# Optimization experiments

Measured on AMD Instinct MI355X. Metric: run time of the kernel, lower is better.

The kernel has to match this reference:

```python
import jax, jax.numpy as jnp
import numpy as np

B, L, D, C = 8, 1024, 512, 4  # batch, maxlen, input_units(=output_unit), channel


def setup_inputs() -> dict:
    key = jax.random.key(0)
    ks = jax.random.split(key, 6)
    scale = 1.0 / np.sqrt(D)  # glorot-ish
    inputs = jax.random.normal(ks[0], (B, L, D), dtype=jnp.float32)
    pad_k = jnp.zeros((B, L, 1), dtype=jnp.float32)  # 0 = valid, -99999 = pad
    w_l = jax.random.normal(ks[1], (C, D, D), dtype=jnp.float32) * scale   # scalar_w per channel
    b_l = jnp.zeros((C,), dtype=jnp.float32)                                # scalar_b per channel
    w_v1 = jax.random.normal(ks[2], (C, D), dtype=jnp.float32) * scale     # vector_w1 [D,1] squeezed
    w_v2 = jax.random.normal(ks[3], (C, D, D), dtype=jnp.float32) * scale  # vector_w2
    b_v = jnp.zeros((C, D), dtype=jnp.float32)                              # vector_b [1,1,D] squeezed
    return {"inputs": inputs, "pad_k": pad_k, "w_l": w_l, "b_l": b_l,
            "w_v1": w_v1, "w_v2": w_v2, "b_v": b_v}


def reference(inputs, pad_k, w_l, b_l, w_v1, w_v2, b_v):
    # inputs: [B,L,D], pad_k: [B,L,1]. Dropout (mask_prob) is identity at inference.
    pad_k2 = (pad_k + 99999.0) / 99999.0              # [B,L,1], 1 at valid, 0 at pad
    pk = pad_k[:, None, :, 0]                          # [B,1,L]

    # --- scalar (pairwise bilinear) attention, all channels at once ---
    mat_l = jnp.einsum('bld,cde->bcle', inputs, w_l)   # [B,C,L,D]
    # M[b,c,i,j] = sum_d inputs[b,i,d] * mat_l[b,c,j,d] + b_l[c]
    M = jnp.einsum('bid,bcjd->bcij', inputs, mat_l) + b_l[None, :, None, None]
    A = jnp.tanh(M)                                    # [B,C,L,L]
    s = A.sum(axis=3)                                  # sum over j -> [B,C,L]
    a = jax.nn.softmax(pk + s, axis=-1)[..., None]     # softmax over L -> [B,C,L,1]

    # --- vector attention ---
    sb = jnp.tanh(jnp.einsum('bld,cde->bcle', inputs, w_v2) + b_v[None, :, None, :])  # [B,C,L,D]
    score_bar = jnp.einsum('bcld,cd->bcl', sb, w_v1) + pk                              # [B,C,L]
    a_bar = jax.nn.softmax(score_bar, axis=-1)                                         # [B,C,L]
    pooled = jnp.einsum('bcl,bld->bcd', a_bar, inputs)                                 # [B,C,D]

    # C_l = a_l * inputs + pooled(broadcast over L) * pad_k2
    C_l = a * inputs[:, None] + pooled[:, :, None, :] * pad_k2[:, None]                # [B,C,L,D]

    C_features = jnp.concatenate(
        [jnp.transpose(C_l, (0, 2, 3, 1)), inputs[..., None]], axis=-1)                # [B,L,D,C+1]
    return C_features, a, a_bar[..., None]
```

## Files before the change

### kernel.cpp

```cpp
#include <hip/hip_runtime.h>

#define BB 8
#define LL 1024
#define DD 512
#define CC 4

typedef unsigned short u16;
typedef unsigned int u32;
typedef __attribute__((ext_vector_type(8))) short bf16x8;
typedef __attribute__((ext_vector_type(4))) float f32x4;
typedef __attribute__((ext_vector_type(4))) unsigned short u16x4;
typedef __attribute__((ext_vector_type(4))) float float4v;

typedef __attribute__((address_space(1))) const u32 gu32;
typedef __attribute__((address_space(3))) u32 lu32;
typedef __attribute__((address_space(3))) u16 l16;

__device__ __forceinline__ void gload16(const void* g, void* l) {
  __builtin_amdgcn_global_load_lds((gu32*)g, (lu32*)l, 16, 0, 0);
}
__device__ __forceinline__ u32 lds_off(const u16* p) {
  return (u32)(uintptr_t)(l16*)p;
}

__device__ __forceinline__ u16 f2bf(float f) {
  unsigned u = __float_as_uint(f);
  u += 0x7FFF + ((u >> 16) & 1);
  return (u16)(u >> 16);
}
__device__ __forceinline__ float bf2f(u16 h) {
  return __uint_as_float(((unsigned)h) << 16);
}
__device__ __forceinline__ float fast_tanh(float x) {
  return 1.0f - 2.0f / (__expf(2.0f * x) + 1.0f);
}

__global__ __launch_bounds__(256) void k_split(const float4v* __restrict__ x,
                                               u16* __restrict__ hi, u16* __restrict__ lo) {
  int i = blockIdx.x * 256 + threadIdx.x;
  float4v v = x[i];
  u16x4 h, l;
#pragma unroll
  for (int k = 0; k < 4; ++k) {
    u16 hh = f2bf(v[k]);
    h[k] = hh;
    l[k] = f2bf(v[k] - bf2f(hh));
  }
  *(u16x4*)&hi[(size_t)i * 4] = h;
  *(u16x4*)&lo[(size_t)i * 4] = l;
}

__global__ __launch_bounds__(256) void k_tsplit(const float* __restrict__ w,
                                                u16* __restrict__ thi, u16* __restrict__ tlo) {
  __shared__ float t[32][33];
  int c = blockIdx.z;
  int tx = threadIdx.x;
  int ty = threadIdx.y;
  int e0 = blockIdx.x * 32, d0 = blockIdx.y * 32;
#pragma unroll
  for (int k = 0; k < 32; k += 8)
    t[ty + k][tx] = w[((size_t)c * DD + d0 + ty + k) * DD + e0 + tx];
  __syncthreads();
#pragma unroll
  for (int k = 0; k < 32; k += 8) {
    float v = t[tx][ty + k];
    size_t o = ((size_t)c * DD + e0 + ty + k) * DD + d0 + tx;
    u16 h = f2bf(v);
    thi[o] = h;
    if (tlo) tlo[o] = f2bf(v - bf2f(h));
  }
}

#define DSR(dst, addr, OFF) \
  asm volatile("ds_read_b128 %0, %1 offset:" #OFF : "=v"(dst) : "v"(addr))
#define LGKM(N) \
  do { __builtin_amdgcn_sched_barrier(0); \
       asm volatile("s_waitcnt lgkmcnt(" #N ")" ::: "memory"); \
       __builtin_amdgcn_sched_barrier(0); } while (0)

template<int NSEG, bool SPLIT>
__device__ __forceinline__ void gemm256(const u16* __restrict__ Ahi, const u16* __restrict__ Alo,
                                        const u16* __restrict__ Bhi, const u16* __restrict__ Blo,
                                        u16* lA, u16* lB, f32x4 (&acc)[8][4]) {
  const int tid = threadIdx.x;
  const int lane = tid & 63;
  const int wave = tid >> 6;
  const int wr = wave >> 2, wc = wave & 3;
  const int fr = lane & 15;
  const int fq = lane >> 4;
  const int srow = tid >> 2;
  const int xs = (tid & 3) ^ ((srow >> 1) & 3);
  const size_t soff = (size_t)srow * DD + (size_t)xs * 8;
  const int sidx = fq ^ ((fr >> 1) & 3);
  const u32 ra = lds_off(lA) + (u32)((wr * 128 + fr) * 64 + sidx * 16);
  const u32 rb = lds_off(lB) + (u32)((wc * 64 + fr) * 64 + sidx * 16);

  const int NT = NSEG * 16;

#define STAGE(t, beo) do {                                                    \
    const int seg_ = SPLIT ? ((t) >> 4) : 0;                                  \
    const int kp_ = ((t) & 15) * 32;                                          \
    const u16* As_ = (SPLIT && seg_ == 1) ? Alo : Ahi;                        \
    const u16* Bs_ = (SPLIT && seg_ == 2) ? Blo : Bhi;                        \
    _Pragma("unroll")                                                         \
    for (int i_ = 0; i_ < 2; ++i_) {                                          \
      gload16(As_ + soff + (size_t)i_ * 128 * DD + kp_,                       \
              lA + (beo) + tid * 8 + i_ * 4096);                              \
      gload16(Bs_ + soff + (size_t)i_ * 128 * DD + kp_,                       \
              lB + (beo) + tid * 8 + i_ * 4096);                              \
    }                                                                         \
  } while (0)

#define MFMA2(m0, m1) do {                                                    \
    _Pragma("unroll")                                                         \
    for (int ni = 0; ni < 4; ++ni)                                            \
      acc[m0][ni] = __builtin_amdgcn_mfma_f32_16x16x32_bf16(                  \
          af[m0], bv[ni], acc[m0][ni], 0, 0, 0);                              \
    _Pragma("unroll")                                                         \
    for (int ni = 0; ni < 4; ++ni)                                            \
      acc[m1][ni] = __builtin_amdgcn_mfma_f32_16x16x32_bf16(                  \
          af[m1], bv[ni], acc[m1][ni], 0, 0, 0);                              \
  } while (0)

#define COMPUTE(bo_) do {                                                     \
    u32 aA_ = ra + (bo_), aB_ = rb + (bo_);                                   \
    bf16x8 af[8], bv[4];                                                      \
    DSR(bv[0], aB_, 0);    DSR(bv[1], aB_, 1024);                             \
    DSR(bv[2], aB_, 2048); DSR(bv[3], aB_, 3072);                             \
    DSR(af[0], aA_, 0);    DSR(af[1], aA_, 1024);                             \
    DSR(af[2], aA_, 2048); DSR(af[3], aA_, 3072);                             \
    LGKM(2);                         \
    __builtin_amdgcn_s_setprio(1);                                            \
    MFMA2(0, 1);                                                              \
    DSR(af[4], aA_, 4096); DSR(af[5], aA_, 5120);                             \
    LGKM(2);                                \
    MFMA2(2, 3);                                                              \
    DSR(af[6], aA_, 6144); DSR(af[7], aA_, 7168);                             \
    LGKM(2);                                \
    MFMA2(4, 5);                                                              \
    LGKM(0);                              \
    MFMA2(6, 7);                                                              \
    __builtin_amdgcn_s_setprio(0);                                            \
    __builtin_amdgcn_s_barrier();            \
  } while (0)

  STAGE(0, 0);
  STAGE(1, 8192);
  int be = 16384;
  u32 bo = 0;
#pragma unroll 1
  for (int t = 0; t < NT - 2; ++t) {
    STAGE(t + 2, be);
    be = (be == 16384) ? 0 : be + 8192;
    __builtin_amdgcn_sched_barrier(0);
    asm volatile("s_waitcnt vmcnt(8)" ::: "memory");
    __builtin_amdgcn_sched_barrier(0);
    __builtin_amdgcn_s_barrier();
    __builtin_amdgcn_sched_barrier(0);
    COMPUTE(bo);
    bo = (bo == 32768u) ? 0u : bo + 16384u;
  }
  __builtin_amdgcn_sched_barrier(0);
  asm volatile("s_waitcnt vmcnt(4)" ::: "memory");
  __builtin_amdgcn_sched_barrier(0);
  __builtin_amdgcn_s_barrier();
  __builtin_amdgcn_sched_barrier(0);
  COMPUTE(bo);
  bo = (bo == 32768u) ? 0u : bo + 16384u;
  __builtin_amdgcn_sched_barrier(0);
  asm volatile("s_waitcnt vmcnt(0)" ::: "memory");
  __builtin_amdgcn_sched_barrier(0);
  __builtin_amdgcn_s_barrier();
  __builtin_amdgcn_sched_barrier(0);
  COMPUTE(bo);
#undef STAGE
#undef COMPUTE
#undef MFMA2
}

__global__ __launch_bounds__(512, 2) void k_matl(const u16* __restrict__ Xhi, const u16* __restrict__ Xlo,
                                                 const u16* __restrict__ Whi, const u16* __restrict__ Wlo,
                                                 u16* __restrict__ mhi, u16* __restrict__ mlo) {
  __shared__ u16 lA[3 * 256 * 32];
  __shared__ u16 lB[3 * 256 * 32];
  int lin = blockIdx.x;
  int virt = (lin & 7) * 32 + (lin >> 3);
  int bc = virt >> 3, rem = virt & 7;
  int tm = rem >> 1, tn = rem & 1;
  int b = bc >> 2, c = bc & 3;
  const u16* Ahi = Xhi + (size_t)b * LL * DD + (size_t)tm * 256 * DD;
  const u16* Alo = Xlo + (size_t)b * LL * DD + (size_t)tm * 256 * DD;
  const u16* Bhi = Whi + (size_t)c * DD * DD + (size_t)tn * 256 * DD;
  const u16* Blo = Wlo + (size_t)c * DD * DD + (size_t)tn * 256 * DD;
  f32x4 acc[8][4];
#pragma unroll
  for (int mi = 0; mi < 8; ++mi)
#pragma unroll
    for (int ni = 0; ni < 4; ++ni) acc[mi][ni] = (f32x4){0.f, 0.f, 0.f, 0.f};
  gemm256<3, true>(Ahi, Alo, Bhi, Blo, lA, lB, acc);

  int lane = threadIdx.x & 63, wave = threadIdx.x >> 6;
  int wr = wave >> 2, wc = wave & 3;
  int rgrp = (lane >> 4) * 4, cidx = lane & 15;
#pragma unroll
  for (int mi = 0; mi < 8; ++mi)
#pragma unroll
    for (int ni = 0; ni < 4; ++ni) {
      int row = tm * 256 + wr * 128 + mi * 16 + rgrp;
      int col = tn * 256 + wc * 64 + ni * 16 + cidx;
#pragma unroll
      for (int j = 0; j < 4; ++j) {
        float v = acc[mi][ni][j];
        size_t o = ((size_t)bc * LL + row + j) * DD + col;
        u16 h = f2bf(v);
        mhi[o] = h;
        mlo[o] = f2bf(v - bf2f(h));
      }
    }
}

__global__ __launch_bounds__(512, 2) void k_s(const u16* __restrict__ Xhi, const u16* __restrict__ Xlo,
                                              const u16* __restrict__ mhi, const u16* __restrict__ mlo,
                                              const float* __restrict__ b_l, float* __restrict__ s_part) {
  __shared__ u16 lA[3 * 256 * 32];
  __shared__ u16 lB[3 * 256 * 32];
  int lin = blockIdx.x;
  int virt = (lin & 7) * 64 + (lin >> 3);
  int bc = virt >> 4, rem = virt & 15;
  int tm = rem >> 2, tn = rem & 3;
  int b = bc >> 2, c = bc & 3;
  const u16* Ahi = Xhi + (size_t)b * LL * DD + (size_t)tm * 256 * DD;
  const u16* Alo = Xlo + (size_t)b * LL * DD + (size_t)tm * 256 * DD;
  const u16* Bhi = mhi + (size_t)bc * LL * DD + (size_t)tn * 256 * DD;
  const u16* Blo = mlo + (size_t)bc * LL * DD + (size_t)tn * 256 * DD;
  f32x4 acc[8][4];
#pragma unroll
  for (int mi = 0; mi < 8; ++mi)
#pragma unroll
    for (int ni = 0; ni < 4; ++ni) acc[mi][ni] = (f32x4){0.f, 0.f, 0.f, 0.f};
  gemm256<3, true>(Ahi, Alo, Bhi, Blo, lA, lB, acc);

  int lane = threadIdx.x & 63, wave = threadIdx.x >> 6;
  int wr = wave >> 2, wc = wave & 3;
  float bl = b_l[c];
  float part[8][4];
#pragma unroll
  for (int mi = 0; mi < 8; ++mi)
#pragma unroll
    for (int j = 0; j < 4; ++j) part[mi][j] = 0.f;
#pragma unroll
  for (int mi = 0; mi < 8; ++mi)
#pragma unroll
    for (int ni = 0; ni < 4; ++ni)
#pragma unroll
      for (int j = 0; j < 4; ++j) part[mi][j] += fast_tanh(acc[mi][ni][j] + bl);
#pragma unroll
  for (int mi = 0; mi < 8; ++mi)
#pragma unroll
    for (int j = 0; j < 4; ++j) {
      float v = part[mi][j];
      v += __shfl_xor(v, 1, 64);
      v += __shfl_xor(v, 2, 64);
      v += __shfl_xor(v, 4, 64);
      v += __shfl_xor(v, 8, 64);
      part[mi][j] = v;
    }
  if ((lane & 15) == 0) {
    int slot = bc * 16 + tn * 4 + wc;
    int rg = (lane >> 4) * 4;
#pragma unroll
    for (int mi = 0; mi < 8; ++mi)
#pragma unroll
      for (int j = 0; j < 4; ++j) {
        int row = tm * 256 + wr * 128 + mi * 16 + rg + j;
        s_part[(size_t)slot * LL + row] = part[mi][j];
      }
  }
}

__global__ __launch_bounds__(512, 2) void k_sbar(const u16* __restrict__ Xhi, const u16* __restrict__ Wv2T,
                                                 const float* __restrict__ b_v, const float* __restrict__ w_v1,
                                                 float* __restrict__ sc_part) {
  __shared__ u16 lA[3 * 256 * 32];
  __shared__ u16 lB[3 * 256 * 32];
  int lin = blockIdx.x;
  int virt = (lin & 7) * 32 + (lin >> 3);
  int bc = virt >> 3, rem = virt & 7;
  int tm = rem >> 1, tn = rem & 1;
  int b = bc >> 2, c = bc & 3;
  const u16* Ahi = Xhi + (size_t)b * LL * DD + (size_t)tm * 256 * DD;
  const u16* Bhi = Wv2T + (size_t)c * DD * DD + (size_t)tn * 256 * DD;
  f32x4 acc[8][4];
#pragma unroll
  for (int mi = 0; mi < 8; ++mi)
#pragma unroll
    for (int ni = 0; ni < 4; ++ni) acc[mi][ni] = (f32x4){0.f, 0.f, 0.f, 0.f};
  gemm256<1, false>(Ahi, nullptr, Bhi, nullptr, lA, lB, acc);

  int lane = threadIdx.x & 63, wave = threadIdx.x >> 6;
  int wr = wave >> 2, wc = wave & 3;
  int cidx = lane & 15;
  float wv[4], bvv[4];
#pragma unroll
  for (int ni = 0; ni < 4; ++ni) {
    int col = tn * 256 + wc * 64 + ni * 16 + cidx;
    wv[ni] = w_v1[c * DD + col];
    bvv[ni] = b_v[c * DD + col];
  }
  float part[8][4];
#pragma unroll
  for (int mi = 0; mi < 8; ++mi)
#pragma unroll
    for (int j = 0; j < 4; ++j) part[mi][j] = 0.f;
#pragma unroll
  for (int mi = 0; mi < 8; ++mi)
#pragma unroll
    for (int ni = 0; ni < 4; ++ni)
#pragma unroll
      for (int j = 0; j < 4; ++j) part[mi][j] += fast_tanh(acc[mi][ni][j] + bvv[ni]) * wv[ni];
#pragma unroll
  for (int mi = 0; mi < 8; ++mi)
#pragma unroll
    for (int j = 0; j < 4; ++j) {
      float v = part[mi][j];
      v += __shfl_xor(v, 1, 64);
      v += __shfl_xor(v, 2, 64);
      v += __shfl_xor(v, 4, 64);
      v += __shfl_xor(v, 8, 64);
      part[mi][j] = v;
    }
  if ((lane & 15) == 0) {
    int slot = bc * 8 + tn * 4 + wc;
    int rg = (lane >> 4) * 4;
#pragma unroll
    for (int mi = 0; mi < 8; ++mi)
#pragma unroll
      for (int j = 0; j < 4; ++j) {
        int row = tm * 256 + wr * 128 + mi * 16 + rg + j;
        sc_part[(size_t)slot * LL + row] = part[mi][j];
      }
  }
}

__device__ __forceinline__ float blk_max(float v, float* red, int tid) {
#pragma unroll
  for (int m = 32; m >= 1; m >>= 1) v = fmaxf(v, __shfl_xor(v, m, 64));
  if ((tid & 63) == 0) red[tid >> 6] = v;
  __syncthreads();
  float r = red[0];
#pragma unroll
  for (int k = 1; k < 16; ++k) r = fmaxf(r, red[k]);
  __syncthreads();
  return r;
}
__device__ __forceinline__ float blk_sum(float v, float* red, int tid) {
#pragma unroll
  for (int m = 32; m >= 1; m >>= 1) v += __shfl_xor(v, m, 64);
  if ((tid & 63) == 0) red[tid >> 6] = v;
  __syncthreads();
  float r = red[0];
#pragma unroll
  for (int k = 1; k < 16; ++k) r += red[k];
  __syncthreads();
  return r;
}

__global__ __launch_bounds__(1024) void k_softmax(const float* __restrict__ s_part,
                                                  const float* __restrict__ sc_part,
                                                  const float* __restrict__ pad_k,
                                                  const float* __restrict__ X,
                                                  float* __restrict__ a_out,
                                                  float* __restrict__ abar_out,
                                                  float* __restrict__ pooled) {
  __shared__ float red[16];
  __shared__ float sm_abar[LL];
  __shared__ float pp[DD];
  int bc = blockIdx.x, b = bc >> 2;
  int i = threadIdx.x;
  float pk = pad_k[b * LL + i];

  float s = pk;
#pragma unroll
  for (int p = 0; p < 16; ++p) s += s_part[(size_t)(bc * 16 + p) * LL + i];
  float mx = blk_max(s, red, i);
  float e = expf(s - mx);
  float sum = blk_sum(e, red, i);
  float a = e / sum;
  a_out[bc * LL + i] = a;

  float sb = pk;
#pragma unroll
  for (int p = 0; p < 8; ++p) sb += sc_part[(size_t)(bc * 8 + p) * LL + i];
  float mx2 = blk_max(sb, red, i);
  float e2 = expf(sb - mx2);
  float sum2 = blk_sum(e2, red, i);
  float ab = e2 / sum2;
  abar_out[bc * LL + i] = ab;
  sm_abar[i] = ab;
  __syncthreads();

  {
    int d = i & (DD - 1), h = i >> 9;
    const float* xb = X + (size_t)b * LL * DD + (size_t)h * 512 * DD + d;
    const float* abp = sm_abar + h * 512;
    float a0 = 0.f, a1 = 0.f, a2 = 0.f, a3 = 0.f;
    for (int l = 0; l < 512; l += 4) {
      a0 += abp[l + 0] * xb[(size_t)(l + 0) * DD];
      a1 += abp[l + 1] * xb[(size_t)(l + 1) * DD];
      a2 += abp[l + 2] * xb[(size_t)(l + 2) * DD];
      a3 += abp[l + 3] * xb[(size_t)(l + 3) * DD];
    }
    float sv = (a0 + a1) + (a2 + a3);
    if (h == 1) pp[d] = sv;
    __syncthreads();
    if (h == 0) pooled[bc * DD + d] = sv + pp[d];
  }
}

__global__ __launch_bounds__(256) void k_assemble(const float* __restrict__ X,
                                                  const float* __restrict__ pad_k,
                                                  const float* __restrict__ a,
                                                  const float* __restrict__ pooled,
                                                  float* __restrict__ out) {
  __shared__ float buf[1280];
  int t = threadIdx.x;
  size_t idx = (size_t)blockIdx.x * 256 + t;
  int d = (int)(idx & (DD - 1));
  int bl = (int)(idx >> 9);
  int b = bl >> 10;
  int l = bl & (LL - 1);
  float x = X[idx];
  float pk2 = (pad_k[bl] + 99999.0f) * (1.0f / 99999.0f);
#pragma unroll
  for (int c = 0; c < 4; ++c) {
    float av = a[(size_t)(b * 4 + c) * LL + l];
    float pv = pooled[(size_t)(b * 4 + c) * DD + d];
    buf[t * 5 + c] = av * x + pv * pk2;
  }
  buf[t * 5 + 4] = x;
  __syncthreads();
  size_t base = (size_t)blockIdx.x * 1280;
#pragma unroll
  for (int k = 0; k < 5; ++k) out[base + k * 256 + t] = buf[k * 256 + t];
}

extern "C" void kernel_launch(void* const* d_in, const int* in_sizes, int n_in,
                              void* d_out, int out_size, void* d_ws, size_t ws_size,
                              hipStream_t stream) {
  (void)in_sizes; (void)n_in; (void)out_size;
  const float* X     = (const float*)d_in[0];
  const float* pad_k = (const float*)d_in[1];
  const float* w_l   = (const float*)d_in[2];
  const float* b_l   = (const float*)d_in[3];
  const float* w_v1  = (const float*)d_in[4];
  const float* w_v2  = (const float*)d_in[5];
  const float* b_v   = (const float*)d_in[6];
  float* out = (float*)d_out;

  char* wsp = (char*)d_ws;
  const size_t NEED = 26279936;
  bool small_ws = ws_size < NEED;
  u16* Xhi = (u16*)wsp;
  u16* Xlo = small_ws ? (u16*)((char*)d_out + 67108864)
                      : (u16*)(wsp + 8388608);
  size_t off = small_ws ? 8388608 : 16777216;
  u16* WlThi = (u16*)(wsp + off);  off += 2097152;
  u16* WlTlo = (u16*)(wsp + off);  off += 2097152;
  u16* Wv2T  = (u16*)(wsp + off);  off += 2097152;
  float* s_part  = (float*)(wsp + off); off += 2097152;
  float* sc_part = (float*)(wsp + off); off += 1048576;
  float* pooled  = (float*)(wsp + off); off += 65536;

  u16* mhi = (u16*)d_out;
  u16* mlo = (u16*)d_out + 16777216;

  float* a_out    = out + 20971520;
  float* abar_out = out + 21004288;

  k_split<<<4096, 256, 0, stream>>>((const float4v*)X, Xhi, Xlo);
  k_tsplit<<<dim3(16, 16, 4), dim3(32, 8), 0, stream>>>(w_l, WlThi, WlTlo);
  k_tsplit<<<dim3(16, 16, 4), dim3(32, 8), 0, stream>>>(w_v2, Wv2T, nullptr);

  k_matl<<<256, 512, 0, stream>>>(Xhi, Xlo, WlThi, WlTlo, mhi, mlo);
  k_s<<<512, 512, 0, stream>>>(Xhi, Xlo, mhi, mlo, b_l, s_part);
  k_sbar<<<256, 512, 0, stream>>>(Xhi, Wv2T, b_v, w_v1, sc_part);

  k_softmax<<<32, 1024, 0, stream>>>(s_part, sc_part, pad_k, X, a_out, abar_out, pooled);
  k_assemble<<<16384, 256, 0, stream>>>(X, pad_k, a_out, pooled, out);
}
```

Before: 244.3 us.

## Interleave half of GEMM prefetch with MFMAs and split pooling into parallel kernel

The GEMM main loop now issues only half of each stage's global-to-LDS loads before the barrier and the other half in the middle of the MFMA sequence. The wait count is adjusted to match, so load issue overlaps with matrix compute instead of bunching up at the top of each iteration. Separately, the attention-weighted pooling over L is moved out of the 32-block softmax kernel into its own 256-block kernel, which spreads the strided reads of X over many more CUs. The cost is one extra kernel launch and a round trip of a_bar through global memory.

```diff
diff --git a/kernel.cpp b/kernel.cpp
--- a/kernel.cpp
+++ b/kernel.cpp
@@ -97,18 +97,15 @@
 
   const int NT = NSEG * 16;
 
-#define STAGE(t, beo) do {                                                    \
+#define STAGE_PAIR(t, beo, half) do {                                         \
     const int seg_ = SPLIT ? ((t) >> 4) : 0;                                  \
     const int kp_ = ((t) & 15) * 32;                                          \
     const u16* As_ = (SPLIT && seg_ == 1) ? Alo : Ahi;                        \
     const u16* Bs_ = (SPLIT && seg_ == 2) ? Blo : Bhi;                        \
-    _Pragma("unroll")                                                         \
-    for (int i_ = 0; i_ < 2; ++i_) {                                          \
-      gload16(As_ + soff + (size_t)i_ * 128 * DD + kp_,                       \
-              lA + (beo) + tid * 8 + i_ * 4096);                              \
-      gload16(Bs_ + soff + (size_t)i_ * 128 * DD + kp_,                       \
-              lB + (beo) + tid * 8 + i_ * 4096);                              \
-    }                                                                         \
+    gload16(As_ + soff + (size_t)(half) * 128 * DD + kp_,                     \
+            lA + (beo) + tid * 8 + (half) * 4096);                            \
+    gload16(Bs_ + soff + (size_t)(half) * 128 * DD + kp_,                     \
+            lB + (beo) + tid * 8 + (half) * 4096);                            \
   } while (0)
 
 #define MFMA2(m0, m1) do {                                                    \
@@ -122,42 +119,63 @@
           af[m1], bv[ni], acc[m1][ni], 0, 0, 0);                              \
   } while (0)
 
-#define COMPUTE(bo_) do {                                                     \
+#define COMPUTE_PEEL(bo_) do {                                                \
     u32 aA_ = ra + (bo_), aB_ = rb + (bo_);                                   \
     bf16x8 af[8], bv[4];                                                      \
     DSR(bv[0], aB_, 0);    DSR(bv[1], aB_, 1024);                             \
     DSR(bv[2], aB_, 2048); DSR(bv[3], aB_, 3072);                             \
     DSR(af[0], aA_, 0);    DSR(af[1], aA_, 1024);                             \
     DSR(af[2], aA_, 2048); DSR(af[3], aA_, 3072);                             \
-    LGKM(2);                         \
+    LGKM(2);                                                                  \
     __builtin_amdgcn_s_setprio(1);                                            \
     MFMA2(0, 1);                                                              \
     DSR(af[4], aA_, 4096); DSR(af[5], aA_, 5120);                             \
-    LGKM(2);                                \
+    LGKM(2);                                                                  \
     MFMA2(2, 3);                                                              \
     DSR(af[6], aA_, 6144); DSR(af[7], aA_, 7168);                             \
-    LGKM(2);                                \
+    LGKM(2);                                                                  \
     MFMA2(4, 5);                                                              \
-    LGKM(0);                              \
+    LGKM(0);                                                                  \
     MFMA2(6, 7);                                                              \
     __builtin_amdgcn_s_setprio(0);                                            \
     __builtin_amdgcn_s_barrier();            \
   } while (0)
 
-  STAGE(0, 0);
-  STAGE(1, 8192);
+  STAGE_PAIR(0, 0, 0);      STAGE_PAIR(0, 0, 1);
+  STAGE_PAIR(1, 8192, 0);   STAGE_PAIR(1, 8192, 1);
   int be = 16384;
   u32 bo = 0;
 #pragma unroll 1
   for (int t = 0; t < NT - 2; ++t) {
-    STAGE(t + 2, be);
-    be = (be == 16384) ? 0 : be + 8192;
+    STAGE_PAIR(t + 2, be, 0);
     __builtin_amdgcn_sched_barrier(0);
-    asm volatile("s_waitcnt vmcnt(8)" ::: "memory");
+    asm volatile("s_waitcnt vmcnt(6)" ::: "memory");
     __builtin_amdgcn_sched_barrier(0);
     __builtin_amdgcn_s_barrier();
     __builtin_amdgcn_sched_barrier(0);
-    COMPUTE(bo);
+    {
+      u32 aA_ = ra + bo, aB_ = rb + bo;
+      bf16x8 af[8], bv[4];
+      DSR(bv[0], aB_, 0);    DSR(bv[1], aB_, 1024);
+      DSR(bv[2], aB_, 2048); DSR(bv[3], aB_, 3072);
+      DSR(af[0], aA_, 0);    DSR(af[1], aA_, 1024);
+      DSR(af[2], aA_, 2048); DSR(af[3], aA_, 3072);
+      LGKM(2);
+      __builtin_amdgcn_s_setprio(1);
+      MFMA2(0, 1);
+      DSR(af[4], aA_, 4096); DSR(af[5], aA_, 5120);
+      LGKM(2);
+      MFMA2(2, 3);
+      STAGE_PAIR(t + 2, be, 1);
+      DSR(af[6], aA_, 6144); DSR(af[7], aA_, 7168);
+      LGKM(2);
+      MFMA2(4, 5);
+      LGKM(0);
+      MFMA2(6, 7);
+      __builtin_amdgcn_s_setprio(0);
+      __builtin_amdgcn_s_barrier();
+    }
+    be = (be == 16384) ? 0 : be + 8192;
     bo = (bo == 32768u) ? 0u : bo + 16384u;
   }
   __builtin_amdgcn_sched_barrier(0);
@@ -165,16 +183,16 @@
   __builtin_amdgcn_sched_barrier(0);
   __builtin_amdgcn_s_barrier();
   __builtin_amdgcn_sched_barrier(0);
-  COMPUTE(bo);
+  COMPUTE_PEEL(bo);
   bo = (bo == 32768u) ? 0u : bo + 16384u;
   __builtin_amdgcn_sched_barrier(0);
   asm volatile("s_waitcnt vmcnt(0)" ::: "memory");
   __builtin_amdgcn_sched_barrier(0);
   __builtin_amdgcn_s_barrier();
   __builtin_amdgcn_sched_barrier(0);
-  COMPUTE(bo);
-#undef STAGE
-#undef COMPUTE
+  COMPUTE_PEEL(bo);
+#undef STAGE_PAIR
+#undef COMPUTE_PEEL
 #undef MFMA2
 }
 
@@ -368,13 +386,9 @@
 __global__ __launch_bounds__(1024) void k_softmax(const float* __restrict__ s_part,
                                                   const float* __restrict__ sc_part,
                                                   const float* __restrict__ pad_k,
-                                                  const float* __restrict__ X,
                                                   float* __restrict__ a_out,
-                                                  float* __restrict__ abar_out,
-                                                  float* __restrict__ pooled) {
+                                                  float* __restrict__ abar_out) {
   __shared__ float red[16];
-  __shared__ float sm_abar[LL];
-  __shared__ float pp[DD];
   int bc = blockIdx.x, b = bc >> 2;
   int i = threadIdx.x;
   float pk = pad_k[b * LL + i];
@@ -385,8 +399,7 @@
   float mx = blk_max(s, red, i);
   float e = expf(s - mx);
   float sum = blk_sum(e, red, i);
-  float a = e / sum;
-  a_out[bc * LL + i] = a;
+  a_out[bc * LL + i] = e / sum;
 
   float sb = pk;
 #pragma unroll
@@ -394,27 +407,29 @@
   float mx2 = blk_max(sb, red, i);
   float e2 = expf(sb - mx2);
   float sum2 = blk_sum(e2, red, i);
-  float ab = e2 / sum2;
-  abar_out[bc * LL + i] = ab;
-  sm_abar[i] = ab;
-  __syncthreads();
-
-  {
-    int d = i & (DD - 1), h = i >> 9;
-    const float* xb = X + (size_t)b * LL * DD + (size_t)h * 512 * DD + d;
-    const float* abp = sm_abar + h * 512;
-    float a0 = 0.f, a1 = 0.f, a2 = 0.f, a3 = 0.f;
-    for (int l = 0; l < 512; l += 4) {
-      a0 += abp[l + 0] * xb[(size_t)(l + 0) * DD];
-      a1 += abp[l + 1] * xb[(size_t)(l + 1) * DD];
-      a2 += abp[l + 2] * xb[(size_t)(l + 2) * DD];
-      a3 += abp[l + 3] * xb[(size_t)(l + 3) * DD];
-    }
-    float sv = (a0 + a1) + (a2 + a3);
-    if (h == 1) pp[d] = sv;
-    __syncthreads();
-    if (h == 0) pooled[bc * DD + d] = sv + pp[d];
-  }
+  abar_out[bc * LL + i] = e2 / sum2;
+}
+
+__global__ __launch_bounds__(256) void k_pool(const float* __restrict__ abar,
+                                              const float* __restrict__ X,
+                                              float* __restrict__ pooled) {
+  __shared__ float pp[256];
+  int bc = blockIdx.x >> 3, dc = blockIdx.x & 7;
+  int b = bc >> 2;
+  int t = threadIdx.x;
+  int d = dc * 64 + (t & 63);
+  int lg = t >> 6;
+  const float* xb = X + (size_t)b * LL * DD + d;
+  const float* ab = abar + (size_t)bc * LL;
+  float s0 = 0.f, s1 = 0.f;
+  for (int l = lg; l < LL; l += 8) {
+    s0 += ab[l] * xb[(size_t)l * DD];
+    s1 += ab[l + 4] * xb[(size_t)(l + 4) * DD];
+  }
+  pp[t] = s0 + s1;
+  __syncthreads();
+  if (t < 64)
+    pooled[bc * DD + dc * 64 + t] = pp[t] + pp[t + 64] + pp[t + 128] + pp[t + 192];
 }
 
 __global__ __launch_bounds__(256) void k_assemble(const float* __restrict__ X,
@@ -485,6 +500,7 @@
   k_s<<<512, 512, 0, stream>>>(Xhi, Xlo, mhi, mlo, b_l, s_part);
   k_sbar<<<256, 512, 0, stream>>>(Xhi, Wv2T, b_v, w_v1, sc_part);
 
-  k_softmax<<<32, 1024, 0, stream>>>(s_part, sc_part, pad_k, X, a_out, abar_out, pooled);
+  k_softmax<<<32, 1024, 0, stream>>>(s_part, sc_part, pad_k, a_out, abar_out);
+  k_pool<<<256, 256, 0, stream>>>(abar_out, X, pooled);
   k_assemble<<<16384, 256, 0, stream>>>(X, pad_k, a_out, pooled, out);
 }
```

New measurement: 260.7 us. 1.07x slower.

## Switch GEMM pipeline to BK=64 double buffer with mid-compute staged loads

Applied to the files above, without the earlier changes.

The shared GEMM core moves from a triple-buffered K=32 pipeline to a double-buffered K=64 pipeline, using a new 8-way XOR LDS swizzle. Each iteration now runs two MFMA halves per barrier. Half of the next tile's global-to-LDS loads are issued in the middle of the first half's MFMA sequence. The goal is to halve the number of barriers and loop iterations and to overlap loads with compute. The cost is less prefetch depth and a larger LDS footprint per block (64KB), which could limit occupancy at 2 blocks per CU.

```diff
diff --git a/kernel.cpp b/kernel.cpp
--- a/kernel.cpp
+++ b/kernel.cpp
@@ -88,27 +88,35 @@
   const int wr = wave >> 2, wc = wave & 3;
   const int fr = lane & 15;
   const int fq = lane >> 4;
-  const int srow = tid >> 2;
-  const int xs = (tid & 3) ^ ((srow >> 1) & 3);
-  const size_t soff = (size_t)srow * DD + (size_t)xs * 8;
-  const int sidx = fq ^ ((fr >> 1) & 3);
-  const u32 ra = lds_off(lA) + (u32)((wr * 128 + fr) * 64 + sidx * 16);
-  const u32 rb = lds_off(lB) + (u32)((wc * 64 + fr) * 64 + sidx * 16);
-
-  const int NT = NSEG * 16;
-
-#define STAGE(t, beo) do {                                                    \
-    const int seg_ = SPLIT ? ((t) >> 4) : 0;                                  \
-    const int kp_ = ((t) & 15) * 32;                                          \
+  const int xs = (tid & 7) ^ ((tid >> 3) & 7);
+  const size_t soff = (size_t)(tid >> 3) * DD + (size_t)xs * 8;
+  const int p0 = fq ^ (fr & 7);
+  const int dk = ((p0 ^ 4) - p0) * 16;
+  const u32 ra = lds_off(lA) + (u32)((wr * 128 + fr) * 128 + p0 * 16);
+  const u32 rb = lds_off(lB) + (u32)((wc * 64 + fr) * 128 + p0 * 16);
+
+  const int NT = NSEG * 8;
+
+#define STAGE_TOP(T, beo) do {                                                \
+    const int seg_ = SPLIT ? ((T) >> 3) : 0;                                  \
+    const int kp_ = ((T) & 7) * 64;                                           \
     const u16* As_ = (SPLIT && seg_ == 1) ? Alo : Ahi;                        \
     const u16* Bs_ = (SPLIT && seg_ == 2) ? Blo : Bhi;                        \
-    _Pragma("unroll")                                                         \
-    for (int i_ = 0; i_ < 2; ++i_) {                                          \
-      gload16(As_ + soff + (size_t)i_ * 128 * DD + kp_,                       \
-              lA + (beo) + tid * 8 + i_ * 4096);                              \
-      gload16(Bs_ + soff + (size_t)i_ * 128 * DD + kp_,                       \
-              lB + (beo) + tid * 8 + i_ * 4096);                              \
-    }                                                                         \
+    gload16(As_ + soff + kp_,                 lA + (beo) + tid * 8);          \
+    gload16(Bs_ + soff + kp_,                 lB + (beo) + tid * 8);          \
+    gload16(As_ + soff + (size_t)64 * DD + kp_, lA + (beo) + tid * 8 + 4096); \
+    gload16(Bs_ + soff + (size_t)64 * DD + kp_, lB + (beo) + tid * 8 + 4096); \
+  } while (0)
+
+#define STAGE_MID(T, beo) do {                                                \
+    const int seg_ = SPLIT ? ((T) >> 3) : 0;                                  \
+    const int kp_ = ((T) & 7) * 64;                                           \
+    const u16* As_ = (SPLIT && seg_ == 1) ? Alo : Ahi;                        \
+    const u16* Bs_ = (SPLIT && seg_ == 2) ? Blo : Bhi;                        \
+    gload16(As_ + soff + (size_t)128 * DD + kp_, lA + (beo) + tid * 8 + 8192);  \
+    gload16(Bs_ + soff + (size_t)128 * DD + kp_, lB + (beo) + tid * 8 + 8192);  \
+    gload16(As_ + soff + (size_t)192 * DD + kp_, lA + (beo) + tid * 8 + 12288); \
+    gload16(Bs_ + soff + (size_t)192 * DD + kp_, lB + (beo) + tid * 8 + 12288); \
   } while (0)
 
 #define MFMA2(m0, m1) do {                                                    \
@@ -122,67 +130,92 @@
           af[m1], bv[ni], acc[m1][ni], 0, 0, 0);                              \
   } while (0)
 
-#define COMPUTE(bo_) do {                                                     \
-    u32 aA_ = ra + (bo_), aB_ = rb + (bo_);                                   \
+#define HALF(aA_, aB_) do {                                                   \
     bf16x8 af[8], bv[4];                                                      \
-    DSR(bv[0], aB_, 0);    DSR(bv[1], aB_, 1024);                             \
-    DSR(bv[2], aB_, 2048); DSR(bv[3], aB_, 3072);                             \
-    DSR(af[0], aA_, 0);    DSR(af[1], aA_, 1024);                             \
-    DSR(af[2], aA_, 2048); DSR(af[3], aA_, 3072);                             \
-    LGKM(2);                         \
-    __builtin_amdgcn_s_setprio(1);                                            \
+    DSR(bv[0], aB_, 0);    DSR(bv[1], aB_, 2048);                             \
+    DSR(bv[2], aB_, 4096); DSR(bv[3], aB_, 6144);                             \
+    DSR(af[0], aA_, 0);    DSR(af[1], aA_, 2048);                             \
+    DSR(af[2], aA_, 4096); DSR(af[3], aA_, 6144);                             \
+    LGKM(2);                                                                  \
     MFMA2(0, 1);                                                              \
-    DSR(af[4], aA_, 4096); DSR(af[5], aA_, 5120);                             \
-    LGKM(2);                                \
+    DSR(af[4], aA_, 8192); DSR(af[5], aA_, 10240);                            \
+    LGKM(2);                                                                  \
     MFMA2(2, 3);                                                              \
-    DSR(af[6], aA_, 6144); DSR(af[7], aA_, 7168);                             \
-    LGKM(2);                                \
+    DSR(af[6], aA_, 12288); DSR(af[7], aA_, 14336);                           \
+    LGKM(2);                                                                  \
     MFMA2(4, 5);                                                              \
-    LGKM(0);                              \
+    LGKM(0);                                                                  \
     MFMA2(6, 7);                                                              \
-    __builtin_amdgcn_s_setprio(0);                                            \
-    __builtin_amdgcn_s_barrier();            \
   } while (0)
 
-  STAGE(0, 0);
-  STAGE(1, 8192);
-  int be = 16384;
+#define HALF_MID(aA_, aB_, T, beo) do {                                       \
+    bf16x8 af[8], bv[4];                                                      \
+    DSR(bv[0], aB_, 0);    DSR(bv[1], aB_, 2048);                             \
+    DSR(bv[2], aB_, 4096); DSR(bv[3], aB_, 6144);                             \
+    DSR(af[0], aA_, 0);    DSR(af[1], aA_, 2048);                             \
+    DSR(af[2], aA_, 4096); DSR(af[3], aA_, 6144);                             \
+    LGKM(2);                                                                  \
+    MFMA2(0, 1);                                                              \
+    DSR(af[4], aA_, 8192); DSR(af[5], aA_, 10240);                            \
+    LGKM(2);                                                                  \
+    MFMA2(2, 3);                                                              \
+    STAGE_MID(T, beo);                                                        \
+    DSR(af[6], aA_, 12288); DSR(af[7], aA_, 14336);                           \
+    LGKM(2);                                                                  \
+    MFMA2(4, 5);                                                              \
+    LGKM(0);                                                                  \
+    MFMA2(6, 7);                                                              \
+  } while (0)
+
+  STAGE_TOP(0, 0);
+  STAGE_MID(0, 0);
+  int beN = 16384;
   u32 bo = 0;
 #pragma unroll 1
-  for (int t = 0; t < NT - 2; ++t) {
-    STAGE(t + 2, be);
-    be = (be == 16384) ? 0 : be + 8192;
+  for (int t = 0; t < NT - 1; ++t) {
+    STAGE_TOP(t + 1, beN);
     __builtin_amdgcn_sched_barrier(0);
-    asm volatile("s_waitcnt vmcnt(8)" ::: "memory");
+    asm volatile("s_waitcnt vmcnt(4)" ::: "memory");
     __builtin_amdgcn_sched_barrier(0);
     __builtin_amdgcn_s_barrier();
     __builtin_amdgcn_sched_barrier(0);
-    COMPUTE(bo);
-    bo = (bo == 32768u) ? 0u : bo + 16384u;
-  }
-  __builtin_amdgcn_sched_barrier(0);
-  asm volatile("s_waitcnt vmcnt(4)" ::: "memory");
-  __builtin_amdgcn_sched_barrier(0);
-  __builtin_amdgcn_s_barrier();
-  __builtin_amdgcn_sched_barrier(0);
-  COMPUTE(bo);
-  bo = (bo == 32768u) ? 0u : bo + 16384u;
+    {
+      u32 aA0 = ra + bo, aB0 = rb + bo;
+      __builtin_amdgcn_s_setprio(1);
+      HALF_MID(aA0, aB0, t + 1, beN);
+      u32 aA1 = aA0 + dk, aB1 = aB0 + dk;
+      HALF(aA1, aB1);
+      __builtin_amdgcn_s_setprio(0);
+      __builtin_amdgcn_s_barrier();
+    }
+    beN ^= 16384;
+    bo ^= 32768u;
+  }
   __builtin_amdgcn_sched_barrier(0);
   asm volatile("s_waitcnt vmcnt(0)" ::: "memory");
   __builtin_amdgcn_sched_barrier(0);
   __builtin_amdgcn_s_barrier();
   __builtin_amdgcn_sched_barrier(0);
-  COMPUTE(bo);
-#undef STAGE
-#undef COMPUTE
+  {
+    u32 aA0 = ra + bo, aB0 = rb + bo;
+    __builtin_amdgcn_s_setprio(1);
+    HALF(aA0, aB0);
+    u32 aA1 = aA0 + dk, aB1 = aB0 + dk;
+    HALF(aA1, aB1);
+    __builtin_amdgcn_s_setprio(0);
+  }
+#undef STAGE_TOP
+#undef STAGE_MID
+#undef HALF
+#undef HALF_MID
 #undef MFMA2
 }
 
 __global__ __launch_bounds__(512, 2) void k_matl(const u16* __restrict__ Xhi, const u16* __restrict__ Xlo,
                                                  const u16* __restrict__ Whi, const u16* __restrict__ Wlo,
                                                  u16* __restrict__ mhi, u16* __restrict__ mlo) {
-  __shared__ u16 lA[3 * 256 * 32];
-  __shared__ u16 lB[3 * 256 * 32];
+  __shared__ u16 lA[2 * 256 * 64];
+  __shared__ u16 lB[2 * 256 * 64];
   int lin = blockIdx.x;
   int virt = (lin & 7) * 32 + (lin >> 3);
   int bc = virt >> 3, rem = virt & 7;
@@ -222,8 +255,8 @@
 __global__ __launch_bounds__(512, 2) void k_s(const u16* __restrict__ Xhi, const u16* __restrict__ Xlo,
                                               const u16* __restrict__ mhi, const u16* __restrict__ mlo,
                                               const float* __restrict__ b_l, float* __restrict__ s_part) {
-  __shared__ u16 lA[3 * 256 * 32];
-  __shared__ u16 lB[3 * 256 * 32];
+  __shared__ u16 lA[2 * 256 * 64];
+  __shared__ u16 lB[2 * 256 * 64];
   int lin = blockIdx.x;
   int virt = (lin & 7) * 64 + (lin >> 3);
   int bc = virt >> 4, rem = virt & 15;
@@ -281,8 +314,8 @@
 __global__ __launch_bounds__(512, 2) void k_sbar(const u16* __restrict__ Xhi, const u16* __restrict__ Wv2T,
                                                  const float* __restrict__ b_v, const float* __restrict__ w_v1,
                                                  float* __restrict__ sc_part) {
-  __shared__ u16 lA[3 * 256 * 32];
-  __shared__ u16 lB[3 * 256 * 32];
+  __shared__ u16 lA[2 * 256 * 64];
+  __shared__ u16 lB[2 * 256 * 64];
   int lin = blockIdx.x;
   int virt = (lin & 7) * 32 + (lin >> 3);
   int bc = virt >> 3, rem = virt & 7;
```

Result: faster. 226.7 us (-7.2%).
